# Kernel tuning notes

Hardware: AMD Instinct MI355X
Metric: run time of the kernel (lower is better)

## Reference

```python
import jax, jax.numpy as jnp
import numpy as np

N, E, DIN, DOUT = 100000, 1000000, 128, 128
C = 1.0            # curvature c_in = c_out = 1.0
EPS = 4e-3         # PoincareBall float32 boundary eps
MIN_NORM = 1e-15
NEG_SLOPE = 0.01   # F.leaky_relu default


def _proj(x, c):
    norm = jnp.maximum(jnp.linalg.norm(x, axis=-1, keepdims=True), MIN_NORM)
    maxnorm = (1.0 - EPS) / jnp.sqrt(c)
    return jnp.where(norm > maxnorm, x / norm * maxnorm, x)


def _expmap0(u, c):
    sqrt_c = jnp.sqrt(c)
    u_norm = jnp.maximum(jnp.linalg.norm(u, axis=-1, keepdims=True), MIN_NORM)
    return jnp.tanh(sqrt_c * u_norm) * u / (sqrt_c * u_norm)


def _mobius_add(x, y, c):
    x2 = jnp.sum(x * x, -1, keepdims=True)
    y2 = jnp.sum(y * y, -1, keepdims=True)
    xy = jnp.sum(x * y, -1, keepdims=True)
    num = (1.0 + 2.0 * c * xy + c * y2) * x + (1.0 - c * x2) * y
    denom = 1.0 + 2.0 * c * xy + c * c * x2 * y2
    return num / jnp.maximum(denom, MIN_NORM)


def _p2k(x, c):  # Poincare ball -> Klein model
    return 2.0 * x / (1.0 + c * jnp.sum(x * x, -1, keepdims=True))


def _k2p(x, c):  # Klein model -> Poincare ball
    denom = 1.0 + jnp.sqrt(jnp.maximum(1.0 - c * jnp.sum(x * x, -1, keepdims=True), MIN_NORM))
    return x / denom


def _lorenz_factor(x, c=1.0):  # 1/sqrt(1 - c||x||^2), keepdim
    return 1.0 / jnp.sqrt(jnp.maximum(1.0 - c * jnp.sum(x * x, -1, keepdims=True), MIN_NORM))


def setup_inputs() -> dict:
    key = jax.random.key(0)
    kx, kr, ko, kw, kb = jax.random.split(key, 5)
    x = 0.1 * jax.random.normal(kx, (N, DIN), dtype=jnp.float32)
    row = jax.random.randint(kr, (E,), 0, N)
    off = jax.random.randint(ko, (E,), 1, N)
    col = (row + off) % N  # guaranteed no self-loops; reference appends them
    edge_index = jnp.stack([row, col]).astype(jnp.int64)
    # geotorch-orthogonal weight in the original; any full-rank matrix is fine for the baseline
    W = jax.random.normal(kw, (DOUT, DIN), dtype=jnp.float32) / np.sqrt(DIN)
    bias = jax.random.uniform(kb, (1, DOUT), dtype=jnp.float32, minval=-0.1, maxval=0.1)
    return {"x": x, "W": W, "bias": bias, "edge_index": edge_index}


def reference(x, W, bias, edge_index):
    row0, col0 = edge_index[0], edge_index[1]
    # add_remaining_self_loops (no self-loops present by construction)
    loop = jnp.arange(N)
    row = jnp.concatenate([row0, loop])
    col = jnp.concatenate([col0, loop])
    w = jnp.ones(row.shape, x.dtype)
    deg = jax.ops.segment_sum(w, row, num_segments=N)
    dinv = jnp.where(deg > 0, deg ** -0.5, 0.0)
    norm = dinv[row] * w * dinv[col]                      # [E+N]

    # HypMPLinear
    h = x @ W.T
    h = _proj(h, C)
    hyp_bias = _expmap0(bias, C)                          # proj_tan0 is identity on Poincare ball
    h = _proj(_mobius_add(h, hyp_bias, C), C)

    # HypMPAgg (agg_type=1)
    s = _p2k(h, C)                                        # [N, D]
    lamb = _lorenz_factor(s)                              # [N, 1], default c=1.0
    support_w = norm[:, None] * lamb[col]                 # [E+N, 1]
    s_j = support_w * s[col]                              # [E+N, D]
    tmp = jax.ops.segment_sum(support_w, row, num_segments=N)   # [N, 1]
    s_out = jax.ops.segment_sum(s_j, row, num_segments=N) / tmp # [N, D]
    out = _k2p(s_out, C)

    # HypMPAct: leaky_relu applied directly
    return jax.nn.leaky_relu(out, NEG_SLOPE)
```

## Files before the change

### kernel.cpp

```cpp
#include <hip/hip_runtime.h>
#include <math.h>


#define EPS_B 4e-3f
#define MINN 1e-15f
#define PAD 40

typedef __bf16 bf16_t;
typedef __attribute__((ext_vector_type(8))) __bf16 bf16x8;
typedef __attribute__((ext_vector_type(4))) __bf16 bf16x4;
typedef __attribute__((ext_vector_type(4))) float f32x4;

#define WP 136
#define HP 140

__global__ __launch_bounds__(256, 2) void k_fused(const float* __restrict__ x,
                                                  const float* __restrict__ W,
                                                  const float* __restrict__ bias,
                                                  const int* __restrict__ row,
                                                  bf16_t* __restrict__ sbuf,
                                                  float* __restrict__ nsbuf,
                                                  float* __restrict__ lambbuf,
                                                  int* __restrict__ cnt,
                                                  int* __restrict__ pos,
                                                  int N, int E, int gb) {
    if (blockIdx.x >= (unsigned)gb) {
        int e = (blockIdx.x - gb) * 256 + threadIdx.x;
        if (e < E) pos[e] = atomicAdd(&cnt[row[e]], 1);
        return;
    }

    __shared__ __align__(16) unsigned char smem[128 * WP * 2 * 2];
    bf16_t* Whi = (bf16_t*)smem;
    bf16_t* Wlo = Whi + 128 * WP;
    float* h_s = (float*)smem;
    __shared__ float hb_s[128];

    const int t = threadIdx.x;
    const int base = blockIdx.x * 64;
    const float MAXN = 1.0f - EPS_B;

    if (t < 128) hb_s[t] = bias[t];
    __syncthreads();
    const int l6 = t & 63;
    float b0 = hb_s[2 * l6], b1 = hb_s[2 * l6 + 1];
    float bn2 = b0 * b0 + b1 * b1;
#pragma unroll
    for (int m = 1; m < 64; m <<= 1) bn2 += __shfl_xor(bn2, m);
    float un = fmaxf(sqrtf(bn2), MINN);
    float th = tanhf(un);
    float y2 = th * th;
    __syncthreads();
    if (t < 128) hb_s[t] *= th / un;

#pragma unroll
    for (int i2 = 0; i2 < 16; ++i2) {
        int idx = t + 256 * i2;
        int r = idx >> 5, c4 = idx & 31;
        float4 v = ((const float4*)W)[idx];
        bf16_t h0 = (bf16_t)v.x, h1 = (bf16_t)v.y, h2 = (bf16_t)v.z, h3 = (bf16_t)v.w;
        bf16x4 hv = {h0, h1, h2, h3};
        bf16x4 lv = {(bf16_t)(v.x - (float)h0), (bf16_t)(v.y - (float)h1),
                     (bf16_t)(v.z - (float)h2), (bf16_t)(v.w - (float)h3)};
        *(bf16x4*)&Whi[r * WP + 4 * c4] = hv;
        *(bf16x4*)&Wlo[r * WP + 4 * c4] = lv;
    }

    const int w = t >> 6, l = t & 63;
    const int mrow = l & 15, kq = l >> 4;
    const int gn = base + 16 * w + mrow;
    bf16x8 ahi[4], alo[4];
    {
        const float4* xr4 = (const float4*)(x + (size_t)gn * 128);
#pragma unroll
        for (int kt = 0; kt < 4; ++kt) {
            float4 v0 = make_float4(0.f, 0.f, 0.f, 0.f), v1 = v0;
            if (gn < N) {
                v0 = xr4[8 * kt + 2 * kq];
                v1 = xr4[8 * kt + 2 * kq + 1];
            }
            float f[8] = {v0.x, v0.y, v0.z, v0.w, v1.x, v1.y, v1.z, v1.w};
#pragma unroll
            for (int i = 0; i < 8; ++i) {
                bf16_t h = (bf16_t)f[i];
                ahi[kt][i] = h;
                alo[kt][i] = (bf16_t)(f[i] - (float)h);
            }
        }
    }
    __syncthreads();

    f32x4 acc[8];
#pragma unroll
    for (int nt = 0; nt < 8; ++nt) acc[nt] = (f32x4){0.f, 0.f, 0.f, 0.f};

#pragma unroll
    for (int nt = 0; nt < 8; ++nt) {
#pragma unroll
        for (int kt = 0; kt < 4; ++kt) {
            bf16x8 bhi = *(bf16x8*)&Whi[(16 * nt + mrow) * WP + 32 * kt + 8 * kq];
            bf16x8 blo = *(bf16x8*)&Wlo[(16 * nt + mrow) * WP + 32 * kt + 8 * kq];
            acc[nt] = __builtin_amdgcn_mfma_f32_16x16x32_bf16(ahi[kt], bhi, acc[nt], 0, 0, 0);
            acc[nt] = __builtin_amdgcn_mfma_f32_16x16x32_bf16(alo[kt], bhi, acc[nt], 0, 0, 0);
            acc[nt] = __builtin_amdgcn_mfma_f32_16x16x32_bf16(ahi[kt], blo, acc[nt], 0, 0, 0);
        }
    }
    __syncthreads();

#pragma unroll
    for (int nt = 0; nt < 8; ++nt)
#pragma unroll
        for (int r = 0; r < 4; ++r)
            h_s[(16 * w + 4 * kq + r) * HP + 16 * nt + mrow] = acc[nt][r];
    __syncthreads();

    const int node = t >> 2, lg = t & 3;
    const int gn2 = base + node;
    float h[32], hb[32];
#pragma unroll
    for (int q = 0; q < 8; ++q) {
        float4 v = *(const float4*)&h_s[node * HP + lg * 32 + 4 * q];
        h[4 * q] = v.x; h[4 * q + 1] = v.y; h[4 * q + 2] = v.z; h[4 * q + 3] = v.w;
        float4 b = *(const float4*)&hb_s[lg * 32 + 4 * q];
        hb[4 * q] = b.x; hb[4 * q + 1] = b.y; hb[4 * q + 2] = b.z; hb[4 * q + 3] = b.w;
    }
    float x2 = 0.f;
#pragma unroll
    for (int d = 0; d < 32; ++d) x2 += h[d] * h[d];
    x2 += __shfl_xor(x2, 1); x2 += __shfl_xor(x2, 2);
    float nrm = sqrtf(x2);
    float sc = nrm > MAXN ? MAXN / nrm : 1.f;
#pragma unroll
    for (int d = 0; d < 32; ++d) h[d] *= sc;
    x2 *= sc * sc;
    float xy = 0.f;
#pragma unroll
    for (int d = 0; d < 32; ++d) xy += h[d] * hb[d];
    xy += __shfl_xor(xy, 1); xy += __shfl_xor(xy, 2);
    float ca = 1.f + 2.f * xy + y2;
    float cb = 1.f - x2;
    float den = 1.f + 2.f * xy + x2 * y2;
    float invd = 1.f / fmaxf(den, MINN);
    float m2 = 0.f;
#pragma unroll
    for (int d = 0; d < 32; ++d) {
        float v = (ca * h[d] + cb * hb[d]) * invd;
        h[d] = v;
        m2 += v * v;
    }
    m2 += __shfl_xor(m2, 1); m2 += __shfl_xor(m2, 2);
    float nrm2 = sqrtf(m2);
    float sc2 = nrm2 > MAXN ? MAXN / nrm2 : 1.f;
    m2 *= sc2 * sc2;
    float pf = 2.f / (1.f + m2);
    float ns = pf * pf * m2;
    float lamb = rsqrtf(fmaxf(1.f - ns, MINN));
    if (gn2 < N) {
        bf16_t* dst = sbuf + (size_t)gn2 * 128 + lg * 32;
        float f = pf * sc2;
#pragma unroll
        for (int q = 0; q < 4; ++q) {
            bf16x8 sv;
#pragma unroll
            for (int j = 0; j < 8; ++j) sv[j] = (bf16_t)(f * h[8 * q + j]);
            *(bf16x8*)&dst[8 * q] = sv;
        }
        if (lg == 0) {
            nsbuf[gn2] = ns;
            lambbuf[gn2] = lamb;
        }
    }
}

__global__ __launch_bounds__(256) void k_place2(const int* __restrict__ row,
                                                const int* __restrict__ col,
                                                const int* __restrict__ pos,
                                                int* __restrict__ csrp, int E) {
    int e = blockIdx.x * 256 + threadIdx.x;
    if (e < E) {
        int p = pos[e];
        if (p < PAD) csrp[(size_t)row[e] * PAD + p] = col[e];
    }
}

__global__ __launch_bounds__(256) void k_g(const float* __restrict__ lamb,
                                           const int* __restrict__ cnt,
                                           float* __restrict__ g, int N) {
    int i = blockIdx.x * 256 + threadIdx.x;
    if (i < N) g[i] = lamb[i] * rsqrtf((float)(cnt[i] + 1));
}

__global__ __launch_bounds__(256) void k_agg(const bf16_t* __restrict__ s,
                                             const float* __restrict__ nsb,
                                             const float* __restrict__ g,
                                             const int* __restrict__ cnt,
                                             const int* __restrict__ csrp,
                                             float* __restrict__ out, int N) {
    const int lane = threadIdx.x & 63, wid = threadIdx.x >> 6;
    const int q = lane >> 4, ql = lane & 15;
    const int i = blockIdx.x * 16 + wid * 4 + q;
    const bool valid = i < N;
    const int ic = valid ? i : 0;

    int c = valid ? cnt[ic] : 0;
    if (c > PAD) c = PAD;
    const float gi = g[ic];
    const size_t st = (size_t)ic * PAD;

    float a[8];
    {
        bf16x8 sv = *(const bf16x8*)(s + (size_t)ic * 128 + ql * 8);
#pragma unroll
        for (int d = 0; d < 8; ++d) a[d] = gi * (float)sv[d];
    }
    float gvs = 0.f;

    for (int bs = 0; bs < c; bs += 16) {
        int rem = c - bs;
        if (rem > 16) rem = 16;
        int jv = 0;
        float gv = 0.f;
        if (ql < rem) {
            jv = csrp[st + bs + ql];
            gv = g[jv];
        }
        gvs += gv;
        for (int e = 0; e < rem; e += 4) {
            int j0 = __shfl(jv, 16 * q + e);
            int j1 = __shfl(jv, 16 * q + e + 1);
            int j2 = __shfl(jv, 16 * q + e + 2);
            int j3 = __shfl(jv, 16 * q + e + 3);
            float g0 = __shfl(gv, 16 * q + e);
            float g1 = __shfl(gv, 16 * q + e + 1);
            float g2 = __shfl(gv, 16 * q + e + 2);
            float g3 = __shfl(gv, 16 * q + e + 3);
            bf16x8 v0 = *(const bf16x8*)(s + (size_t)j0 * 128 + ql * 8);
            bf16x8 v1 = *(const bf16x8*)(s + (size_t)j1 * 128 + ql * 8);
            bf16x8 v2 = *(const bf16x8*)(s + (size_t)j2 * 128 + ql * 8);
            bf16x8 v3 = *(const bf16x8*)(s + (size_t)j3 * 128 + ql * 8);
#pragma unroll
            for (int d = 0; d < 8; ++d) {
                a[d] = fmaf(g0, (float)v0[d], a[d]);
                a[d] = fmaf(g1, (float)v1[d], a[d]);
                a[d] = fmaf(g2, (float)v2[d], a[d]);
                a[d] = fmaf(g3, (float)v3[d], a[d]);
            }
        }
    }
    gvs += __shfl_xor(gvs, 1); gvs += __shfl_xor(gvs, 2);
    gvs += __shfl_xor(gvs, 4); gvs += __shfl_xor(gvs, 8);
    float tw = gi + gvs;

    float inv = 1.f / tw;
    float o[8];
    float ns = 0.f;
#pragma unroll
    for (int d = 0; d < 8; ++d) {
        o[d] = a[d] * inv;
        ns += o[d] * o[d];
    }
    ns += __shfl_xor(ns, 1); ns += __shfl_xor(ns, 2);
    ns += __shfl_xor(ns, 4); ns += __shfl_xor(ns, 8);
    if (c == 0) ns = nsb[ic];
    float den = 1.f + sqrtf(fmaxf(1.f - ns, MINN));
    float id = 1.f / den;
#pragma unroll
    for (int d = 0; d < 8; ++d) {
        float v = o[d] * id;
        o[d] = v >= 0.f ? v : 0.01f * v;
    }
    if (valid) {
        float* dst = out + (size_t)i * 128 + ql * 8;
        *(float4*)dst = make_float4(o[0], o[1], o[2], o[3]);
        *(float4*)(dst + 4) = make_float4(o[4], o[5], o[6], o[7]);
    }
}

extern "C" void kernel_launch(void* const* d_in, const int* in_sizes, int n_in,
                              void* d_out, int out_size, void* d_ws, size_t ws_size,
                              hipStream_t stream) {
    const float* x    = (const float*)d_in[0];
    const float* W    = (const float*)d_in[1];
    const float* bias = (const float*)d_in[2];
    const int*   ei   = (const int*)d_in[3];

    const int N = in_sizes[0] / 128;
    const int E = in_sizes[3] / 2;
    const int* row = ei;
    const int* col = ei + E;

    float*  g_buf  = (float*)d_ws;
    float*  ns_buf = g_buf + N;
    float*  lambb  = ns_buf + N;
    int*    cnt    = (int*)(lambb + N);
    int*    pos    = cnt + N;
    int*    csrp   = pos + E;
    bf16_t* s_buf  = (bf16_t*)(csrp + (size_t)N * PAD);

    hipMemsetAsync(cnt, 0, (size_t)N * sizeof(int), stream);

    const int gb = (N + 63) / 64;
    const int db = (E + 255) / 256;
    k_fused<<<gb + db, 256, 0, stream>>>(x, W, bias, row, s_buf, ns_buf, lambb,
                                         cnt, pos, N, E, gb);
    k_place2<<<(E + 255) / 256, 256, 0, stream>>>(row, col, pos, csrp, E);
    k_g<<<(N + 255) / 256, 256, 0, stream>>>(lambb, cnt, g_buf, N);
    k_agg<<<(N + 15) / 16, 256, 0, stream>>>(s_buf, ns_buf, g_buf, cnt, csrp,
                                             (float*)d_out, N);
}
```

Before: 140.0 us.

## Split degree counting from GEMM, drop W low-part MFMA, fuse place and g kernels

Moves the atomic degree counting out of the fused GEMM kernel into its own kernel, and merges the CSR placement and per-node g computation into one launch. The GEMM now keeps only the bf16 high part of W, so each tile issues two MFMAs instead of three and shared memory holds half as much. The W padding changes from 136 to 140. Dropping the W low part lowers GEMM precision, and splitting the kernels gives up the overlap between the atomics and the GEMM.

```diff
diff --git a/kernel.cpp b/kernel.cpp
--- a/kernel.cpp
+++ b/kernel.cpp
@@ -11,28 +11,45 @@
 typedef __attribute__((ext_vector_type(4))) __bf16 bf16x4;
 typedef __attribute__((ext_vector_type(4))) float f32x4;
 
-#define WP 136
+#define WP 140
 #define HP 140
 
-__global__ __launch_bounds__(256, 2) void k_fused(const float* __restrict__ x,
-                                                  const float* __restrict__ W,
-                                                  const float* __restrict__ bias,
-                                                  const int* __restrict__ row,
-                                                  bf16_t* __restrict__ sbuf,
-                                                  float* __restrict__ nsbuf,
-                                                  float* __restrict__ lambbuf,
-                                                  int* __restrict__ cnt,
-                                                  int* __restrict__ pos,
-                                                  int N, int E, int gb) {
-    if (blockIdx.x >= (unsigned)gb) {
-        int e = (blockIdx.x - gb) * 256 + threadIdx.x;
-        if (e < E) pos[e] = atomicAdd(&cnt[row[e]], 1);
-        return;
-    }
-
-    __shared__ __align__(16) unsigned char smem[128 * WP * 2 * 2];
-    bf16_t* Whi = (bf16_t*)smem;
-    bf16_t* Wlo = Whi + 128 * WP;
+__global__ __launch_bounds__(256) void k_deg2(const int* __restrict__ row,
+                                              int* __restrict__ cnt,
+                                              int* __restrict__ pos, int E) {
+    int e = blockIdx.x * 256 + threadIdx.x;
+    if (e < E) pos[e] = atomicAdd(&cnt[row[e]], 1);
+}
+
+__global__ __launch_bounds__(256) void k_place2g(const int* __restrict__ row,
+                                                 const int* __restrict__ col,
+                                                 const int* __restrict__ pos,
+                                                 int* __restrict__ csrp,
+                                                 const float* __restrict__ lamb,
+                                                 const int* __restrict__ cnt,
+                                                 float* __restrict__ g,
+                                                 int E, int N, int eb) {
+    if (blockIdx.x < (unsigned)eb) {
+        int e = blockIdx.x * 256 + threadIdx.x;
+        if (e < E) {
+            int p = pos[e];
+            if (p < PAD) csrp[(size_t)row[e] * PAD + p] = col[e];
+        }
+    } else {
+        int i = (blockIdx.x - eb) * 256 + threadIdx.x;
+        if (i < N) g[i] = lamb[i] * rsqrtf((float)(cnt[i] + 1));
+    }
+}
+
+__global__ __launch_bounds__(256, 2) void k_gemm(const float* __restrict__ x,
+                                                 const float* __restrict__ W,
+                                                 const float* __restrict__ bias,
+                                                 bf16_t* __restrict__ sbuf,
+                                                 float* __restrict__ nsbuf,
+                                                 float* __restrict__ lambbuf,
+                                                 int N) {
+    __shared__ __align__(16) unsigned char smem[128 * WP * 2];
+    bf16_t* Wb = (bf16_t*)smem;
     float* h_s = (float*)smem;
     __shared__ float hb_s[128];
 
@@ -58,12 +75,8 @@
         int idx = t + 256 * i2;
         int r = idx >> 5, c4 = idx & 31;
         float4 v = ((const float4*)W)[idx];
-        bf16_t h0 = (bf16_t)v.x, h1 = (bf16_t)v.y, h2 = (bf16_t)v.z, h3 = (bf16_t)v.w;
-        bf16x4 hv = {h0, h1, h2, h3};
-        bf16x4 lv = {(bf16_t)(v.x - (float)h0), (bf16_t)(v.y - (float)h1),
-                     (bf16_t)(v.z - (float)h2), (bf16_t)(v.w - (float)h3)};
-        *(bf16x4*)&Whi[r * WP + 4 * c4] = hv;
-        *(bf16x4*)&Wlo[r * WP + 4 * c4] = lv;
+        bf16x4 hv = {(bf16_t)v.x, (bf16_t)v.y, (bf16_t)v.z, (bf16_t)v.w};
+        *(bf16x4*)&Wb[r * WP + 4 * c4] = hv;
     }
 
     const int w = t >> 6, l = t & 63;
@@ -98,11 +111,9 @@
     for (int nt = 0; nt < 8; ++nt) {
 #pragma unroll
         for (int kt = 0; kt < 4; ++kt) {
-            bf16x8 bhi = *(bf16x8*)&Whi[(16 * nt + mrow) * WP + 32 * kt + 8 * kq];
-            bf16x8 blo = *(bf16x8*)&Wlo[(16 * nt + mrow) * WP + 32 * kt + 8 * kq];
-            acc[nt] = __builtin_amdgcn_mfma_f32_16x16x32_bf16(ahi[kt], bhi, acc[nt], 0, 0, 0);
-            acc[nt] = __builtin_amdgcn_mfma_f32_16x16x32_bf16(alo[kt], bhi, acc[nt], 0, 0, 0);
-            acc[nt] = __builtin_amdgcn_mfma_f32_16x16x32_bf16(ahi[kt], blo, acc[nt], 0, 0, 0);
+            bf16x8 bw = *(bf16x8*)&Wb[(16 * nt + mrow) * WP + 32 * kt + 8 * kq];
+            acc[nt] = __builtin_amdgcn_mfma_f32_16x16x32_bf16(ahi[kt], bw, acc[nt], 0, 0, 0);
+            acc[nt] = __builtin_amdgcn_mfma_f32_16x16x32_bf16(alo[kt], bw, acc[nt], 0, 0, 0);
         }
     }
     __syncthreads();
@@ -170,24 +181,6 @@
             lambbuf[gn2] = lamb;
         }
     }
-}
-
-__global__ __launch_bounds__(256) void k_place2(const int* __restrict__ row,
-                                                const int* __restrict__ col,
-                                                const int* __restrict__ pos,
-                                                int* __restrict__ csrp, int E) {
-    int e = blockIdx.x * 256 + threadIdx.x;
-    if (e < E) {
-        int p = pos[e];
-        if (p < PAD) csrp[(size_t)row[e] * PAD + p] = col[e];
-    }
-}
-
-__global__ __launch_bounds__(256) void k_g(const float* __restrict__ lamb,
-                                           const int* __restrict__ cnt,
-                                           float* __restrict__ g, int N) {
-    int i = blockIdx.x * 256 + threadIdx.x;
-    if (i < N) g[i] = lamb[i] * rsqrtf((float)(cnt[i] + 1));
 }
 
 __global__ __launch_bounds__(256) void k_agg(const bf16_t* __restrict__ s,
@@ -299,12 +292,12 @@
 
     hipMemsetAsync(cnt, 0, (size_t)N * sizeof(int), stream);
 
-    const int gb = (N + 63) / 64;
-    const int db = (E + 255) / 256;
-    k_fused<<<gb + db, 256, 0, stream>>>(x, W, bias, row, s_buf, ns_buf, lambb,
-                                         cnt, pos, N, E, gb);
-    k_place2<<<(E + 255) / 256, 256, 0, stream>>>(row, col, pos, csrp, E);
-    k_g<<<(N + 255) / 256, 256, 0, stream>>>(lambb, cnt, g_buf, N);
+    const int eb = (E + 255) / 256;
+    const int gbk = (N + 255) / 256;
+    k_deg2<<<eb, 256, 0, stream>>>(row, cnt, pos, E);
+    k_gemm<<<(N + 63) / 64, 256, 0, stream>>>(x, W, bias, s_buf, ns_buf, lambb, N);
+    k_place2g<<<eb + gbk, 256, 0, stream>>>(row, col, pos, csrp, lambb, cnt,
+                                            g_buf, E, N, eb);
     k_agg<<<(N + 15) / 16, 256, 0, stream>>>(s_buf, ns_buf, g_buf, cnt, csrp,
                                              (float*)d_out, N);
 }
```

After: 152.0 us. 8.6% more time.
